# Kernel tuning notes

Measured on AMD Instinct MI355X. Metric: run time of the kernel, lower is better.

## Reference

```python
import jax, jax.numpy as jnp
import numpy as np

B, T, I, H = 64, 2048, 64, 256


def setup_inputs() -> dict:
    key = jax.random.key(0)
    ks = jax.random.split(key, 7)
    s_ih = 1.0 / np.sqrt(H)
    return {
        "x": jax.random.normal(ks[0], (B, T, I), dtype=jnp.float32),
        "W_ih": jax.random.normal(ks[1], (H, I), dtype=jnp.float32) * s_ih,
        "W_hh": jax.random.normal(ks[2], (H, H), dtype=jnp.float32) * s_ih,
        "b_ih": jax.random.normal(ks[3], (H,), dtype=jnp.float32) * s_ih,
        "b_hh": jax.random.normal(ks[4], (H,), dtype=jnp.float32) * s_ih,
        "W_fc": jax.random.normal(ks[5], (1, H), dtype=jnp.float32) * s_ih,
        "b_fc": jax.random.normal(ks[6], (1,), dtype=jnp.float32) * s_ih,
    }


def reference(x, W_ih, W_hh, b_ih, b_hh, W_fc, b_fc):
    # Precompute input projection for all timesteps: [B,T,H]
    pre = jnp.einsum('bti,hi->bth', x, W_ih) + b_ih + b_hh
    pre_t = jnp.swapaxes(pre, 0, 1)  # [T,B,H]

    def step(h, p_t):
        h_new = jnp.tanh(p_t + h @ W_hh.T)
        return h_new, h_new

    h0 = jnp.zeros((x.shape[0], W_hh.shape[0]), dtype=x.dtype)
    _, hs = jax.lax.scan(step, h0, pre_t)  # hs: [T,B,H]
    out = jnp.swapaxes(hs, 0, 1)  # [B,T,H]
    return out @ W_fc.T + b_fc  # [B,T,1]
```

## Files before the change

kernel.cpp:

```cpp
#include <hip/hip_runtime.h>

#define BB 64
#define TT 2048
#define II 64
#define HH 256

typedef __fp16 h2_t __attribute__((ext_vector_type(2)));
typedef __fp16 h8_t __attribute__((ext_vector_type(8)));

#define H2(i) __builtin_bit_cast(h2_t, (i))
#define I32(h) __builtin_bit_cast(int, (h))

#if __has_builtin(__builtin_amdgcn_fdot2)
#define FDOT2(a, b, c) __builtin_amdgcn_fdot2((a), (b), (c), false)
#else
__device__ __forceinline__ float FDOT2(h2_t a, h2_t b, float c) {
    return fmaf((float)a[0], (float)b[0], fmaf((float)a[1], (float)b[1], c));
}
#endif

__device__ __forceinline__ float ftanh(float x) {
    float e = __expf(2.0f * x);
    return 1.0f - 2.0f * __builtin_amdgcn_rcpf(e + 1.0f);
}

template <int CTRL>
__device__ __forceinline__ float dpp_add(float v) {
    int s = __builtin_amdgcn_update_dpp(0, __float_as_int(v), CTRL, 0xF, 0xF, true);
    return v + __int_as_float(s);
}
template <int CTRL>
__device__ __forceinline__ float dpp_get(float v) {
    int s = __builtin_amdgcn_update_dpp(0, __float_as_int(v), CTRL, 0xF, 0xF, true);
    return __int_as_float(s);
}
template <int PAT>
__device__ __forceinline__ float swz_get(float v) {
    return __int_as_float(__builtin_amdgcn_ds_swizzle(__float_as_int(v), PAT));
}
template <int PAT>
__device__ __forceinline__ float swz_add(float v) { return v + swz_get<PAT>(v); }

__device__ __forceinline__ float mrg4(float a, float b, int lane) {
    float t = (lane & 4) ? b : a;
    float u = (lane & 4) ? a : b;
    return t + swz_get<0x101F>(u);
}
__device__ __forceinline__ float mrg2(float a, float b, int lane) {
    float t = (lane & 2) ? b : a;
    float u = (lane & 2) ? a : b;
    return t + dpp_get<0x4E>(u);
}
__device__ __forceinline__ float mrg1(float a, float b, int lane) {
    float t = (lane & 1) ? b : a;
    float u = (lane & 1) ? a : b;
    return t + dpp_get<0xB1>(u);
}

__launch_bounds__(256, 1)
__global__ void rnn_fused(const float* __restrict__ x,
                          const float* __restrict__ W_ih,
                          const float* __restrict__ W_hh,
                          const float* __restrict__ b_ih,
                          const float* __restrict__ b_hh,
                          const float* __restrict__ W_fc,
                          const float* __restrict__ b_fc,
                          float* __restrict__ out) {
    __shared__ __align__(16) __fp16 hbuf[2][320];
    __shared__ float part[TT][8];

    const int tid  = threadIdx.x;
    const int b    = blockIdx.x;
    const int lane = tid & 63;
    const int w    = tid >> 6;
    const int o    = lane >> 3;
    const int q    = lane & 7;

    int whh_i[8][16];
    int wih_i[8][4];
#pragma unroll
    for (int r = 0; r < 8; ++r) {
        const int t_r = w * 64 + o * 8 + r;
        const float4* wr = (const float4*)(W_hh + t_r * HH + q * 32);
#pragma unroll
        for (int jv = 0; jv < 8; ++jv) {
            const float4 wv = wr[jv];
            whh_i[r][jv * 2 + 0] = I32(__builtin_amdgcn_cvt_pkrtz(wv.x, wv.y));
            whh_i[r][jv * 2 + 1] = I32(__builtin_amdgcn_cvt_pkrtz(wv.z, wv.w));
        }
        const float4* wi = (const float4*)(W_ih + t_r * II + q * 8);
        const float4 wa = wi[0], wb = wi[1];
        wih_i[r][0] = I32(__builtin_amdgcn_cvt_pkrtz(wa.x, wa.y));
        wih_i[r][1] = I32(__builtin_amdgcn_cvt_pkrtz(wa.z, wa.w));
        wih_i[r][2] = I32(__builtin_amdgcn_cvt_pkrtz(wb.x, wb.y));
        wih_i[r][3] = I32(__builtin_amdgcn_cvt_pkrtz(wb.z, wb.w));
    }
#pragma unroll
    for (int j = 0; j < 128; ++j) asm volatile("" : "+v"(((int*)whh_i)[j]));
#pragma unroll
    for (int j = 0; j < 32; ++j) asm volatile("" : "+v"(((int*)wih_i)[j]));

    const int myrow = w * 64 + lane;
    const float bias = b_ih[myrow] + b_hh[myrow];
    const float wfc  = W_fc[myrow];
    const float bfc  = b_fc[0];

    for (int idx = tid; idx < 2 * 320; idx += 256) ((__fp16*)hbuf)[idx] = (__fp16)0.0f;
    __syncthreads();

    const float* xbase = x + (size_t)b * TT * II + q * 8;
    float* outb = out + (size_t)b * TT;

    const int hoff = (w * 2 + (lane >> 5)) * 80 + (lane & 31) * 2;
    __fp16* hw0 = (__fp16*)((char*)&hbuf[0][0] + hoff);
    __fp16* hw1 = (__fp16*)((char*)&hbuf[1][0] + hoff);

    h2_t xc[4];
    {
        const float4* xp = (const float4*)(xbase);
        const float4 a = xp[0], c = xp[1];
        xc[0] = __builtin_amdgcn_cvt_pkrtz(a.x, a.y);
        xc[1] = __builtin_amdgcn_cvt_pkrtz(a.z, a.w);
        xc[2] = __builtin_amdgcn_cvt_pkrtz(c.x, c.y);
        xc[3] = __builtin_amdgcn_cvt_pkrtz(c.z, c.w);
    }

    int p = 0;
    for (int i = 0; i < TT; ++i) {
        const int rown = (i + 1 < TT) ? (i + 1) : (TT - 1);
        const float4* xpn = (const float4*)(xbase + rown * II);
        const float4 xna = xpn[0], xnc = xpn[1];

        float a0 = 0, a1 = 0, a2 = 0, a3 = 0, a4 = 0, a5 = 0, a6 = 0, a7 = 0;
        const h8_t* hp = (const h8_t*)((const char*)&hbuf[p][0] + q * 80);
#pragma unroll
        for (int jv = 0; jv < 4; ++jv) {
            const h8_t hv = hp[jv];
#pragma unroll
            for (int e = 0; e < 4; ++e) {
                const h2_t hh2 = __builtin_shufflevector(hv, hv, 0, 1);
                const h2_t he = (e == 0) ? __builtin_shufflevector(hv, hv, 0, 1)
                              : (e == 1) ? __builtin_shufflevector(hv, hv, 2, 3)
                              : (e == 2) ? __builtin_shufflevector(hv, hv, 4, 5)
                                         : __builtin_shufflevector(hv, hv, 6, 7);
                const int j = jv * 4 + e;
                a0 = FDOT2(H2(whh_i[0][j]), he, a0);
                a1 = FDOT2(H2(whh_i[1][j]), he, a1);
                a2 = FDOT2(H2(whh_i[2][j]), he, a2);
                a3 = FDOT2(H2(whh_i[3][j]), he, a3);
                a4 = FDOT2(H2(whh_i[4][j]), he, a4);
                a5 = FDOT2(H2(whh_i[5][j]), he, a5);
                a6 = FDOT2(H2(whh_i[6][j]), he, a6);
                a7 = FDOT2(H2(whh_i[7][j]), he, a7);
                (void)hh2;
            }
        }
#pragma unroll
        for (int e = 0; e < 4; ++e) {
            a0 = FDOT2(H2(wih_i[0][e]), xc[e], a0);
            a1 = FDOT2(H2(wih_i[1][e]), xc[e], a1);
            a2 = FDOT2(H2(wih_i[2][e]), xc[e], a2);
            a3 = FDOT2(H2(wih_i[3][e]), xc[e], a3);
            a4 = FDOT2(H2(wih_i[4][e]), xc[e], a4);
            a5 = FDOT2(H2(wih_i[5][e]), xc[e], a5);
            a6 = FDOT2(H2(wih_i[6][e]), xc[e], a6);
            a7 = FDOT2(H2(wih_i[7][e]), xc[e], a7);
        }

        xc[0] = __builtin_amdgcn_cvt_pkrtz(xna.x, xna.y);
        xc[1] = __builtin_amdgcn_cvt_pkrtz(xna.z, xna.w);
        xc[2] = __builtin_amdgcn_cvt_pkrtz(xnc.x, xnc.y);
        xc[3] = __builtin_amdgcn_cvt_pkrtz(xnc.z, xnc.w);

        const float A0 = mrg4(a0, a4, lane);
        const float A1 = mrg4(a1, a5, lane);
        const float A2 = mrg4(a2, a6, lane);
        const float A3 = mrg4(a3, a7, lane);
        const float B0 = mrg2(A0, A2, lane);
        const float B1 = mrg2(A1, A3, lane);
        const float C0 = mrg1(B0, B1, lane);

        const float hn = ftanh(C0 + bias);
        const int pn = p ^ 1;
        if (pn) hw1[0] = (__fp16)hn; else hw0[0] = (__fp16)hn;

        float c = hn * wfc;
        c = dpp_add<0xB1>(c);
        c = dpp_add<0x4E>(c);
        c = swz_add<0x101F>(c);
        c = dpp_add<0x140>(c);
        c = swz_add<0x401F>(c);
        if ((lane & 31) == 0) part[i][w * 2 + (lane >> 5)] = c;

        __syncthreads();
        p = pn;
    }

    for (int i = tid; i < TT; i += 256) {
        const float4* pp = (const float4*)&part[i][0];
        const float4 s0 = pp[0], s1 = pp[1];
        outb[i] = s0.x + s0.y + s0.z + s0.w + s1.x + s1.y + s1.z + s1.w + bfc;
    }
}

extern "C" void kernel_launch(void* const* d_in, const int* in_sizes, int n_in,
                              void* d_out, int out_size, void* d_ws, size_t ws_size,
                              hipStream_t stream) {
    const float* x    = (const float*)d_in[0];
    const float* W_ih = (const float*)d_in[1];
    const float* W_hh = (const float*)d_in[2];
    const float* b_ih = (const float*)d_in[3];
    const float* b_hh = (const float*)d_in[4];
    const float* W_fc = (const float*)d_in[5];
    const float* b_fc = (const float*)d_in[6];
    float* out = (float*)d_out;

    rnn_fused<<<BB, 256, 0, stream>>>(x, W_ih, W_hh, b_ih, b_hh, W_fc, b_fc, out);
}
```

Baseline: 1.319 ms.

## Unroll recurrence by two, defer output reduction, and prefetch inputs further ahead

The time loop is unrolled by two with fixed ping-pong buffer pointers, so the per-step branch on buffer parity goes away. The FC output reduction for step i is moved into step i+1, after the h loads are issued, so it overlaps LDS latency instead of sitting on the critical path before the barrier. DPP row operations replace ds_swizzle in that reduction. x is prefetched two steps ahead using rotating registers, and __syncthreads is replaced by an explicit lgkmcnt wait plus s_barrier. This costs more registers and adds a shifted indexing scheme for the partial-sum array.

```diff
diff --git a/kernel.cpp b/kernel.cpp
--- a/kernel.cpp
+++ b/kernel.cpp
@@ -38,8 +38,6 @@
 __device__ __forceinline__ float swz_get(float v) {
     return __int_as_float(__builtin_amdgcn_ds_swizzle(__float_as_int(v), PAT));
 }
-template <int PAT>
-__device__ __forceinline__ float swz_add(float v) { return v + swz_get<PAT>(v); }
 
 __device__ __forceinline__ float mrg4(float a, float b, int lane) {
     float t = (lane & 4) ? b : a;
@@ -67,7 +65,7 @@
                           const float* __restrict__ b_fc,
                           float* __restrict__ out) {
     __shared__ __align__(16) __fp16 hbuf[2][320];
-    __shared__ float part[TT][8];
+    __shared__ float part[TT + 1][8];
 
     const int tid  = threadIdx.x;
     const int b    = blockIdx.x;
@@ -114,8 +112,11 @@
     const int hoff = (w * 2 + (lane >> 5)) * 80 + (lane & 31) * 2;
     __fp16* hw0 = (__fp16*)((char*)&hbuf[0][0] + hoff);
     __fp16* hw1 = (__fp16*)((char*)&hbuf[1][0] + hoff);
+    const h8_t* hp0 = (const h8_t*)((const char*)&hbuf[0][0] + q * 80);
+    const h8_t* hp1 = (const h8_t*)((const char*)&hbuf[1][0] + q * 80);
 
     h2_t xc[4];
+    float4 sAa, sAc, sBa, sBc;
     {
         const float4* xp = (const float4*)(xbase);
         const float4 a = xp[0], c = xp[1];
@@ -123,81 +124,108 @@
         xc[1] = __builtin_amdgcn_cvt_pkrtz(a.z, a.w);
         xc[2] = __builtin_amdgcn_cvt_pkrtz(c.x, c.y);
         xc[3] = __builtin_amdgcn_cvt_pkrtz(c.z, c.w);
-    }
-
-    int p = 0;
-    for (int i = 0; i < TT; ++i) {
-        const int rown = (i + 1 < TT) ? (i + 1) : (TT - 1);
-        const float4* xpn = (const float4*)(xbase + rown * II);
-        const float4 xna = xpn[0], xnc = xpn[1];
-
-        float a0 = 0, a1 = 0, a2 = 0, a3 = 0, a4 = 0, a5 = 0, a6 = 0, a7 = 0;
-        const h8_t* hp = (const h8_t*)((const char*)&hbuf[p][0] + q * 80);
-#pragma unroll
-        for (int jv = 0; jv < 4; ++jv) {
-            const h8_t hv = hp[jv];
-#pragma unroll
-            for (int e = 0; e < 4; ++e) {
-                const h2_t hh2 = __builtin_shufflevector(hv, hv, 0, 1);
-                const h2_t he = (e == 0) ? __builtin_shufflevector(hv, hv, 0, 1)
-                              : (e == 1) ? __builtin_shufflevector(hv, hv, 2, 3)
-                              : (e == 2) ? __builtin_shufflevector(hv, hv, 4, 5)
-                                         : __builtin_shufflevector(hv, hv, 6, 7);
-                const int j = jv * 4 + e;
-                a0 = FDOT2(H2(whh_i[0][j]), he, a0);
-                a1 = FDOT2(H2(whh_i[1][j]), he, a1);
-                a2 = FDOT2(H2(whh_i[2][j]), he, a2);
-                a3 = FDOT2(H2(whh_i[3][j]), he, a3);
-                a4 = FDOT2(H2(whh_i[4][j]), he, a4);
-                a5 = FDOT2(H2(whh_i[5][j]), he, a5);
-                a6 = FDOT2(H2(whh_i[6][j]), he, a6);
-                a7 = FDOT2(H2(whh_i[7][j]), he, a7);
-                (void)hh2;
-            }
-        }
-#pragma unroll
-        for (int e = 0; e < 4; ++e) {
-            a0 = FDOT2(H2(wih_i[0][e]), xc[e], a0);
-            a1 = FDOT2(H2(wih_i[1][e]), xc[e], a1);
-            a2 = FDOT2(H2(wih_i[2][e]), xc[e], a2);
-            a3 = FDOT2(H2(wih_i[3][e]), xc[e], a3);
-            a4 = FDOT2(H2(wih_i[4][e]), xc[e], a4);
-            a5 = FDOT2(H2(wih_i[5][e]), xc[e], a5);
-            a6 = FDOT2(H2(wih_i[6][e]), xc[e], a6);
-            a7 = FDOT2(H2(wih_i[7][e]), xc[e], a7);
-        }
-
-        xc[0] = __builtin_amdgcn_cvt_pkrtz(xna.x, xna.y);
-        xc[1] = __builtin_amdgcn_cvt_pkrtz(xna.z, xna.w);
-        xc[2] = __builtin_amdgcn_cvt_pkrtz(xnc.x, xnc.y);
-        xc[3] = __builtin_amdgcn_cvt_pkrtz(xnc.z, xnc.w);
-
-        const float A0 = mrg4(a0, a4, lane);
-        const float A1 = mrg4(a1, a5, lane);
-        const float A2 = mrg4(a2, a6, lane);
-        const float A3 = mrg4(a3, a7, lane);
-        const float B0 = mrg2(A0, A2, lane);
-        const float B1 = mrg2(A1, A3, lane);
-        const float C0 = mrg1(B0, B1, lane);
-
-        const float hn = ftanh(C0 + bias);
-        const int pn = p ^ 1;
-        if (pn) hw1[0] = (__fp16)hn; else hw0[0] = (__fp16)hn;
-
-        float c = hn * wfc;
+        const float4* x1 = (const float4*)(xbase + II);
+        sAa = x1[0]; sAc = x1[1];
+        const float4* x2 = (const float4*)(xbase + 2 * II);
+        sBa = x2[0]; sBc = x2[1];
+    }
+
+    float hn_prev = 0.0f;
+
+#define STEP(IDX, HPIN, HWOUT, SA, SC)                                         \
+    {                                                                          \
+          \
+        const h8_t hv0 = (HPIN)[0], hv1 = (HPIN)[1];                           \
+        const h8_t hv2 = (HPIN)[2], hv3 = (HPIN)[3];                           \
+           \
+        {                                                                      \
+            float c = hn_prev * wfc;                                           \
+            c = dpp_add<0xB1>(c);                                      \
+            c = dpp_add<0x4E>(c);                                      \
+            c = dpp_add<0x141>(c);                \
+            c = dpp_add<0x140>(c);                     \
+            c = dpp_add<0x142>(c);    \
+            if ((lane & 31) == 16) part[IDX][w * 2 + (lane >> 5)] = c;         \
+        }                                                                      \
+                 \
+        float a0 = 0, a1 = 0, a2 = 0, a3 = 0, a4 = 0, a5 = 0, a6 = 0, a7 = 0;  \
+        _Pragma("unroll")                                                      \
+        for (int jv = 0; jv < 4; ++jv) {                                       \
+            const h8_t hv = (jv == 0) ? hv0 : (jv == 1) ? hv1                  \
+                          : (jv == 2) ? hv2 : hv3;                             \
+            _Pragma("unroll")                                                  \
+            for (int e = 0; e < 4; ++e) {                                      \
+                const h2_t he = (e == 0) ? __builtin_shufflevector(hv, hv, 0, 1) \
+                              : (e == 1) ? __builtin_shufflevector(hv, hv, 2, 3) \
+                              : (e == 2) ? __builtin_shufflevector(hv, hv, 4, 5) \
+                                         : __builtin_shufflevector(hv, hv, 6, 7); \
+                const int j = jv * 4 + e;                                      \
+                a0 = FDOT2(H2(whh_i[0][j]), he, a0);                           \
+                a1 = FDOT2(H2(whh_i[1][j]), he, a1);                           \
+                a2 = FDOT2(H2(whh_i[2][j]), he, a2);                           \
+                a3 = FDOT2(H2(whh_i[3][j]), he, a3);                           \
+                a4 = FDOT2(H2(whh_i[4][j]), he, a4);                           \
+                a5 = FDOT2(H2(whh_i[5][j]), he, a5);                           \
+                a6 = FDOT2(H2(whh_i[6][j]), he, a6);                           \
+                a7 = FDOT2(H2(whh_i[7][j]), he, a7);                           \
+            }                                                                  \
+        }                                                                      \
+        _Pragma("unroll")                                                      \
+        for (int e = 0; e < 4; ++e) {                                          \
+            a0 = FDOT2(H2(wih_i[0][e]), xc[e], a0);                            \
+            a1 = FDOT2(H2(wih_i[1][e]), xc[e], a1);                            \
+            a2 = FDOT2(H2(wih_i[2][e]), xc[e], a2);                            \
+            a3 = FDOT2(H2(wih_i[3][e]), xc[e], a3);                            \
+            a4 = FDOT2(H2(wih_i[4][e]), xc[e], a4);                            \
+            a5 = FDOT2(H2(wih_i[5][e]), xc[e], a5);                            \
+            a6 = FDOT2(H2(wih_i[6][e]), xc[e], a6);                            \
+            a7 = FDOT2(H2(wih_i[7][e]), xc[e], a7);                            \
+        }                                                                      \
+         \
+        xc[0] = __builtin_amdgcn_cvt_pkrtz((SA).x, (SA).y);                    \
+        xc[1] = __builtin_amdgcn_cvt_pkrtz((SA).z, (SA).w);                    \
+        xc[2] = __builtin_amdgcn_cvt_pkrtz((SC).x, (SC).y);                    \
+        xc[3] = __builtin_amdgcn_cvt_pkrtz((SC).z, (SC).w);                    \
+        {                                                                      \
+            const int rn = ((IDX) + 3 < TT) ? ((IDX) + 3) : (TT - 1);          \
+            const float4* xp = (const float4*)(xbase + rn * II);               \
+            (SA) = xp[0]; (SC) = xp[1];                                        \
+        }                                                                      \
+         \
+        const float A0 = mrg4(a0, a4, lane);                                   \
+        const float A1 = mrg4(a1, a5, lane);                                   \
+        const float A2 = mrg4(a2, a6, lane);                                   \
+        const float A3 = mrg4(a3, a7, lane);                                   \
+        const float B0 = mrg2(A0, A2, lane);                                   \
+        const float B1 = mrg2(A1, A3, lane);                                   \
+        const float C0 = mrg1(B0, B1, lane);                                   \
+        const float hn = ftanh(C0 + bias);                                     \
+        (HWOUT)[0] = (__fp16)hn;                                               \
+        hn_prev = hn;                                                          \
+           \
+                             \
+        asm volatile("s_waitcnt lgkmcnt(0)\n\ts_barrier" ::: "memory");        \
+    }
+
+    for (int ib = 0; ib < TT; ib += 2) {
+        STEP(ib, hp0, hw1, sAa, sAc)
+        STEP(ib + 1, hp1, hw0, sBa, sBc)
+    }
+#undef STEP
+
+    {
+        float c = hn_prev * wfc;
         c = dpp_add<0xB1>(c);
         c = dpp_add<0x4E>(c);
-        c = swz_add<0x101F>(c);
+        c = dpp_add<0x141>(c);
         c = dpp_add<0x140>(c);
-        c = swz_add<0x401F>(c);
-        if ((lane & 31) == 0) part[i][w * 2 + (lane >> 5)] = c;
-
-        __syncthreads();
-        p = pn;
-    }
+        c = dpp_add<0x142>(c);
+        if ((lane & 31) == 16) part[TT][w * 2 + (lane >> 5)] = c;
+    }
+    __syncthreads();
 
     for (int i = tid; i < TT; i += 256) {
-        const float4* pp = (const float4*)&part[i][0];
+        const float4* pp = (const float4*)&part[i + 1][0];
         const float4 s0 = pp[0], s1 = pp[1];
         outb[i] = s0.x + s0.y + s0.z + s0.w + s1.x + s1.y + s1.z + s1.w + bfc;
     }
```

Result: faster. 1.171 ms (-11.2%).
